# Kernel tuning notes

Hardware: AMD Instinct MI355X
Metric: run time of the kernel (lower is better)

The kernel has to match this reference:

```python
import jax, jax.numpy as jnp
import numpy as np

BETA = 8.0  # cfg.memory.beta (inverse temperature)
EPS = 1e-12  # matches F.normalize default eps


def _l2_normalize(x):
    return x / jnp.maximum(jnp.linalg.norm(x, axis=-1, keepdims=True), EPS)


def setup_inputs() -> dict:
    key = jax.random.key(0)
    k1, k2, k3 = jax.random.split(key, 3)
    embeddings = jax.random.normal(k1, (1024, 128), dtype=jnp.float32)   # queries [B, D]
    keys = jax.random.normal(k2, (100000, 128), dtype=jnp.float32)       # stored patterns [N, D]
    labels = jax.random.randint(k3, (100000,), 0, 1000)                  # class per stored pattern [N]
    return {"embeddings": embeddings, "keys": keys, "labels": labels, "n_classes": 1000}


def reference(embeddings, keys, labels, n_classes):
    # store(): keys normalized (normalize_keys=True); values = one_hot(labels)
    k = _l2_normalize(keys)
    # query(): normalize queries, cosine sims, softmax(beta*sims), weighted value sum
    q = _l2_normalize(embeddings)
    sims = q @ k.T                                   # [B, N]
    weights = jax.nn.softmax(BETA * sims, axis=-1)   # [B, N]
    # weights @ one_hot(labels, C) == segment-sum of weights by key label (same math,
    # avoids materializing the dense [N, C] one-hot value matrix)
    out = jax.ops.segment_sum(weights.T, labels, num_segments=n_classes).T  # [B, C]
    return out
```

## Files before the change

### kernel.cpp

```cpp
#include <hip/hip_runtime.h>
#include <math.h>

typedef _Float16 f16;
typedef _Float16 f16x8 __attribute__((ext_vector_type(8)));
typedef float    f32x16 __attribute__((ext_vector_type(16)));
typedef unsigned int uint;
typedef unsigned short u16;

#define B_Q     1024
#define DIM     128
#define N_KEYS  100000
#define NPAD    102400
#define NGP     (NPAD / 32)
#define GPC     16
#define NCHUNK  (NGP / GPC)
#define N_CLS   1000
#define QSCALE  11.541560327111707f
#define NH      128
#define QGRP    (B_Q / 32)
#define ZFLOATS ((N_CLS + 2) * B_Q)

__global__ void k_hist(const int* __restrict__ labels, uint* __restrict__ hist128) {
    __shared__ uint lh[N_CLS];
    for (int i = threadIdx.x; i < N_CLS; i += blockDim.x) lh[i] = 0;
    __syncthreads();
    const int stride = gridDim.x * blockDim.x;
    for (int i = blockIdx.x * blockDim.x + threadIdx.x; i < N_KEYS; i += stride)
        atomicAdd(&lh[labels[i]], 1u);
    __syncthreads();
    for (int i = threadIdx.x; i < N_CLS; i += blockDim.x)
        hist128[blockIdx.x * N_CLS + i] = lh[i];
}

__global__ __launch_bounds__(1024)
void k_scan(const uint* __restrict__ hist128, uint* __restrict__ cursor) {
    __shared__ uint wtot[16];
    const int t = threadIdx.x;
    const int w = t >> 6, lane = t & 63;
    uint v = 0;
    if (t < N_CLS)
        for (int b = 0; b < NH; ++b) v += hist128[b * N_CLS + t];
    uint s = v;
    #pragma unroll
    for (int o = 1; o < 64; o <<= 1) {
        const uint x = __shfl_up(s, o);
        if (lane >= o) s += x;
    }
    if (lane == 63) wtot[w] = s;
    __syncthreads();
    if (w == 0) {
        uint ws = (lane < 16) ? wtot[lane] : 0;
        #pragma unroll
        for (int o = 1; o < 16; o <<= 1) {
            const uint x = __shfl_up(ws, o);
            if (lane >= o) ws += x;
        }
        if (lane < 16) wtot[lane] = ws;
    }
    __syncthreads();
    const uint prefix = (w > 0) ? wtot[w - 1] : 0;
    if (t < N_CLS) cursor[t] = prefix + s - v;
}

__global__ void k_perm(const int* __restrict__ labels, uint* __restrict__ cursor,
                       int* __restrict__ src, u16* __restrict__ kcls) {
    const int n = blockIdx.x * blockDim.x + threadIdx.x;
    if (n >= NPAD) return;
    if (n < N_KEYS) {
        const int lab = labels[n];
        const int pos = (int)atomicAdd(&cursor[lab], 1u);
        src[pos]  = n;
        kcls[pos] = (u16)lab;
    } else {
        src[n]  = -1;
        kcls[n] = (u16)N_CLS;
    }
}

__global__ __launch_bounds__(256)
void k_gather(const float* __restrict__ qm, const float* __restrict__ km,
              const int* __restrict__ src, const u16* __restrict__ kcls,
              f16* __restrict__ kf2, f16* __restrict__ qf2,
              int* __restrict__ meta, float* __restrict__ zbase) {
    __shared__ float ssq[8][32];
    __shared__ float scale[32];
    const int g = blockIdx.x;
    const int t = threadIdx.x;
    const int r = t & 31;
    const int p = t >> 5;
    const bool isq = g >= NGP;

    {
        const int zi = g * 256 + t;
        if (zi < ZFLOATS / 4)
            ((float4*)zbase)[zi] = float4{0.f, 0.f, 0.f, 0.f};
    }

    if (!isq && t < 64) {
        const int  cl = kcls[g * 32 + (t & 31)];
        const int  ca = __shfl(cl, 0);
        const uint dm = (uint)(__ballot(cl != ca) & 0xffffffffull);
        const int  split = dm ? (__ffs(dm) - 1) : 32;
        const int  cb = (split < 32) ? __shfl(cl, split) : ca;
        if (t == 0) meta[g] = ca | (cb << 11) | (split << 22);
    }

    const float* srow;
    if (isq) srow = qm + (size_t)((g - NGP) * 32 + r) * DIM;
    else {
        const int sr = src[g * 32 + r];
        srow = (sr >= 0) ? km + (size_t)sr * DIM : nullptr;
    }

    float4 v[4];
    float ss = 0.0f;
    if (srow) {
        #pragma unroll
        for (int i = 0; i < 4; ++i) {
            v[i] = *(const float4*)(srow + p * 16 + i * 4);
            ss += v[i].x * v[i].x + v[i].y * v[i].y
                + v[i].z * v[i].z + v[i].w * v[i].w;
        }
    } else {
        #pragma unroll
        for (int i = 0; i < 4; ++i) v[i] = float4{0.f, 0.f, 0.f, 0.f};
    }
    ssq[p][r] = ss;
    __syncthreads();
    if (t < 32) {
        float s = 0.0f;
        #pragma unroll
        for (int i = 0; i < 8; ++i) s += ssq[i][t];
        scale[t] = (isq ? QSCALE : 1.0f) / fmaxf(sqrtf(s), 1e-12f);
    }
    __syncthreads();
    const float sc = scale[r];

    const float f[16] = {v[0].x, v[0].y, v[0].z, v[0].w,
                         v[1].x, v[1].y, v[1].z, v[1].w,
                         v[2].x, v[2].y, v[2].z, v[2].w,
                         v[3].x, v[3].y, v[3].z, v[3].w};
    f16x8 h0, h1;
    #pragma unroll
    for (int j = 0; j < 8; ++j) {
        h0[j] = (f16)(f[j]     * sc);
        h1[j] = (f16)(f[j + 8] * sc);
    }
    f16* dst = isq ? qf2 + (size_t)(g - NGP) * 4096
                   : kf2 + (size_t)g * 4096;
    *(f16x8*)(dst + p * 512 +       r * 8) = h0;
    *(f16x8*)(dst + p * 512 + 256 + r * 8) = h1;
}

#define FLUSH2(C) {                                                           \
        const float v0 = racc0 + __shfl_xor(racc0, 32);                       \
        const float v1 = racc1 + __shfl_xor(racc1, 32);                       \
        if ((C) != N_CLS) { tot0 += racc0; tot1 += racc1; }                   \
        if (lhi == 0) {                                                       \
            atomicAdd(&out_t[(size_t)(C) * B_Q + q00 + l31], v0);             \
            atomicAdd(&out_t[(size_t)(C) * B_Q + q01 + l31], v1);             \
        }                                                                     \
    }

#define LOADK(DST, I) {                                                       \
        const f16* _kb = kf2 + (size_t)(g0 + (I)) * 4096 + lane * 8;          \
        _Pragma("unroll")                                                     \
        for (int kk = 0; kk < 8; ++kk) DST[kk] = *(const f16x8*)(_kb + kk * 512); \
    }

#define BODY(KB, I) {                                                         \
        const int m     = __shfl(mv, (I));                                    \
        const int ca    = m & 0x7FF;                                          \
        const int cb    = (m >> 11) & 0x7FF;                                  \
        const int split = m >> 22;                                            \
        f32x16 c0 = {}, c1 = {};                                              \
        _Pragma("unroll")                                                     \
        for (int kk = 0; kk < 8; ++kk) {                                      \
            c0 = __builtin_amdgcn_mfma_f32_32x32x16_f16(KB[kk], Q0[kk], c0, 0, 0, 0); \
            c1 = __builtin_amdgcn_mfma_f32_32x32x16_f16(KB[kk], Q1[kk], c1, 0, 0, 0); \
        }                                                                     \
        if (ca != cur) {                                                      \
            if (cur >= 0) FLUSH2(cur);                                        \
            racc0 = 0.0f; racc1 = 0.0f;                                       \
            cur = ca;                                                         \
        }                                                                     \
        if (split == 32) {                                                    \
            float ga = 0.f, gb = 0.f, gc = 0.f, gd = 0.f;                     \
            _Pragma("unroll")                                                 \
            for (int r = 0; r < 16; r += 2) {                                 \
                ga += __builtin_amdgcn_exp2f(c0[r]);                          \
                gb += __builtin_amdgcn_exp2f(c0[r + 1]);                      \
                gc += __builtin_amdgcn_exp2f(c1[r]);                          \
                gd += __builtin_amdgcn_exp2f(c1[r + 1]);                      \
            }                                                                 \
            racc0 += ga + gb;                                                 \
            racc1 += gc + gd;                                                 \
        } else {                                                              \
            float ga = 0.f, gb = 0.f, gc = 0.f, gd = 0.f;                     \
            float ha = 0.f, hb = 0.f, hc = 0.f, hd = 0.f;                     \
            _Pragma("unroll")                                                 \
            for (int r = 0; r < 16; r += 2) {                                 \
                const int  kr0 = ((r & 3) + 8 * (r >> 2)) + lhi4;             \
                const int  kr1 = (((r + 1) & 3) + 8 * ((r + 1) >> 2)) + lhi4; \
                const float e0  = __builtin_amdgcn_exp2f(c0[r]);              \
                const float e0b = __builtin_amdgcn_exp2f(c0[r + 1]);          \
                const float e1  = __builtin_amdgcn_exp2f(c1[r]);              \
                const float e1b = __builtin_amdgcn_exp2f(c1[r + 1]);          \
                const bool inA0 = kr0 < split;                                \
                const bool inA1 = kr1 < split;                                \
                ga += inA0 ? e0  : 0.0f;  ha += inA0 ? 0.0f : e0;             \
                gb += inA1 ? e0b : 0.0f;  hb += inA1 ? 0.0f : e0b;            \
                gc += inA0 ? e1  : 0.0f;  hc += inA0 ? 0.0f : e1;             \
                gd += inA1 ? e1b : 0.0f;  hd += inA1 ? 0.0f : e1b;            \
            }                                                                 \
            racc0 += ga + gb;                                                 \
            racc1 += gc + gd;                                                 \
            FLUSH2(cur);                                                      \
            racc0 = ha + hb;                                                  \
            racc1 = hc + hd;                                                  \
            cur = cb;                                                         \
        }                                                                     \
    }

__global__ __launch_bounds__(64)
void class_gemm8(const f16* __restrict__ kf2, const f16* __restrict__ qf2,
                 const int* __restrict__ meta, float* __restrict__ out_t,
                 float* __restrict__ qtot) {
    const int lane = threadIdx.x & 63;
    const int l31  = lane & 31;
    const int lhi  = lane >> 5;
    const int lhi4 = lhi << 2;

    const int b     = blockIdx.x;
    const int xcd   = b & 7;
    const int u     = b >> 3;
    const int chunk = xcd * (NCHUNK / 8) + (u >> 4);
    const int qquad = (u >> 2) & 3;
    const int wsub  = u & 3;
    const int g0    = chunk * GPC;

    f16x8 Q0[8], Q1[8];
    {
        const f16* qa = qf2 + (size_t)(qquad * 8 + wsub * 2) * 4096 + lane * 8;
        #pragma unroll
        for (int kk = 0; kk < 8; ++kk) {
            Q0[kk] = *(const f16x8*)(qa + kk * 512);
            Q1[kk] = *(const f16x8*)(qa + 4096 + kk * 512);
        }
    }
    const int q00 = qquad * 256 + wsub * 64;
    const int q01 = q00 + 32;

    const int mv = meta[g0 + (lane & 15)];

    float racc0 = 0.0f, racc1 = 0.0f;
    float tot0  = 0.0f, tot1  = 0.0f;
    int cur = -1;

    f16x8 K0[8], K1[8];
    LOADK(K0, 0);
    #pragma unroll 1
    for (int ii = 0; ii < GPC / 2; ++ii) {
        const int i0 = 2 * ii, i1 = 2 * ii + 1;
        LOADK(K1, i1);
        BODY(K0, i0);
        if (ii + 1 < GPC / 2) LOADK(K0, i1 + 1);
        BODY(K1, i1);
    }
    if (cur >= 0) FLUSH2(cur);

    {
        const float t0 = tot0 + __shfl_xor(tot0, 32);
        const float t1 = tot1 + __shfl_xor(tot1, 32);
        if (lhi == 0) {
            atomicAdd(&qtot[q00 + l31], t0);
            atomicAdd(&qtot[q01 + l31], t1);
        }
    }
}

__global__ __launch_bounds__(256)
void k_norm_t(const float* __restrict__ out_t, const float* __restrict__ qtot,
              float* __restrict__ out) {
    __shared__ float tile[64 * 65];
    __shared__ float invq[64];
    const int tid  = threadIdx.x;
    const int w    = tid >> 6;
    const int lane = tid & 63;
    const int q0   = blockIdx.x * 64;
    const int c0   = blockIdx.y * 64;

    if (tid < 64) invq[tid] = 1.0f / qtot[q0 + tid];

    #pragma unroll
    for (int i = 0; i < 16; ++i) {
        const int cidx = c0 + w * 16 + i;
        const float v = (cidx < N_CLS) ? out_t[(size_t)cidx * B_Q + q0 + lane] : 0.0f;
        tile[lane * 65 + w * 16 + i] = v;
    }
    __syncthreads();
    #pragma unroll
    for (int j = 0; j < 16; ++j) {
        const int r    = w * 16 + j;
        const int cidx = c0 + lane;
        if (cidx < N_CLS)
            out[(size_t)(q0 + r) * N_CLS + cidx] = tile[r * 65 + lane] * invq[r];
    }
}

extern "C" void kernel_launch(void* const* d_in, const int* in_sizes, int n_in,
                              void* d_out, int out_size, void* d_ws, size_t ws_size,
                              hipStream_t stream) {
    const float* qm     = (const float*)d_in[0];
    const float* km     = (const float*)d_in[1];
    const int*   labels = (const int*)d_in[2];
    float* out = (float*)d_out;

    char* p = (char*)d_ws;
    f16*   kf2     = (f16*)p;   p += (size_t)NPAD * DIM * 2;
    f16*   qf2     = (f16*)p;   p += (size_t)B_Q * DIM * 2;
    float* out_t   = (float*)p; p += (size_t)N_CLS * B_Q * 4;
    float* sink    = (float*)p; p += (size_t)B_Q * 4;
    float* qtot    = (float*)p; p += (size_t)B_Q * 4;
    uint*  cursor  = (uint*)p;  p += N_CLS * 4;
    u16*   kcls    = (u16*)p;   p += (size_t)NPAD * 2;
    int*   meta    = (int*)p;   p += (size_t)NGP * 4;
    int*   src     = (int*)p;   p += (size_t)NPAD * 4;
    (void)sink;
    uint*  hist128 = (uint*)out_t;

    hipLaunchKernelGGL(k_hist, dim3(NH), dim3(256), 0, stream, labels, hist128);
    hipLaunchKernelGGL(k_scan, dim3(1), dim3(1024), 0, stream, hist128, cursor);
    hipLaunchKernelGGL(k_perm, dim3(NPAD / 256), dim3(256), 0, stream,
                       labels, cursor, src, kcls);
    hipLaunchKernelGGL(k_gather, dim3(NGP + QGRP), dim3(256), 0, stream,
                       qm, km, src, kcls, kf2, qf2, meta, out_t);

    hipLaunchKernelGGL(class_gemm8, dim3(16 * NCHUNK), dim3(64), 0, stream,
                       kf2, qf2, meta, out_t, qtot);

    hipLaunchKernelGGL(k_norm_t, dim3(B_Q / 64, (N_CLS + 63) / 64), dim3(256), 0, stream,
                       out_t, qtot, out);
}
```

Measured before the change: 103.0 us.

## Halve key-group chunk size, fully unroll, and defer class merge after MFMA loop

Key groups per chunk drop from 16 to 8, which doubles the grid of the class GEMM kernel. The loop is fully unrolled into a straight-line load/compute schedule. The branchy per-group exp/accumulate with interleaved atomic flushes is replaced by a branch-free split sum that stores lo/hi partials in registers. The class-run merge and atomic flushes then run in a separate pass after all MFMAs finish, so the MFMA pipeline no longer stalls on divergent flush code. The cost is more atomics from the doubled chunk count, which means more partial flushes per class boundary, plus higher register use for the partial arrays.

```diff
diff --git a/kernel.cpp b/kernel.cpp
--- a/kernel.cpp
+++ b/kernel.cpp
@@ -12,7 +12,7 @@
 #define N_KEYS  100000
 #define NPAD    102400
 #define NGP     (NPAD / 32)
-#define GPC     16
+#define GPC     8
 #define NCHUNK  (NGP / GPC)
 #define N_CLS   1000
 #define QSCALE  11.541560327111707f
@@ -95,7 +95,6 @@
         if (zi < ZFLOATS / 4)
             ((float4*)zbase)[zi] = float4{0.f, 0.f, 0.f, 0.f};
     }
-
     if (!isq && t < 64) {
         const int  cl = kcls[g * 32 + (t & 31)];
         const int  ca = __shfl(cl, 0);
@@ -169,61 +168,52 @@
     }
 
 #define BODY(KB, I) {                                                         \
-        const int m     = __shfl(mv, (I));                                    \
-        const int ca    = m & 0x7FF;                                          \
-        const int cb    = (m >> 11) & 0x7FF;                                  \
-        const int split = m >> 22;                                            \
+        const int split = __shfl(mv, (I)) >> 22;                              \
         f32x16 c0 = {}, c1 = {};                                              \
         _Pragma("unroll")                                                     \
         for (int kk = 0; kk < 8; ++kk) {                                      \
             c0 = __builtin_amdgcn_mfma_f32_32x32x16_f16(KB[kk], Q0[kk], c0, 0, 0, 0); \
             c1 = __builtin_amdgcn_mfma_f32_32x32x16_f16(KB[kk], Q1[kk], c1, 0, 0, 0); \
         }                                                                     \
+        float la = 0.f, lb = 0.f, lc = 0.f, ld = 0.f;                         \
+        float ta = 0.f, tb = 0.f, tc = 0.f, td = 0.f;                         \
+        _Pragma("unroll")                                                     \
+        for (int r = 0; r < 16; r += 2) {                                     \
+            const int  kr0 = ((r & 3) + 8 * (r >> 2)) + lhi4;                 \
+            const int  kr1 = (((r + 1) & 3) + 8 * ((r + 1) >> 2)) + lhi4;     \
+            const float e0  = __builtin_amdgcn_exp2f(c0[r]);                  \
+            const float e0b = __builtin_amdgcn_exp2f(c0[r + 1]);              \
+            const float e1  = __builtin_amdgcn_exp2f(c1[r]);                  \
+            const float e1b = __builtin_amdgcn_exp2f(c1[r + 1]);              \
+            ta += e0;  tb += e0b;  tc += e1;  td += e1b;                      \
+            la += (kr0 < split) ? e0  : 0.0f;                                 \
+            lb += (kr1 < split) ? e0b : 0.0f;                                 \
+            lc += (kr0 < split) ? e1  : 0.0f;                                 \
+            ld += (kr1 < split) ? e1b : 0.0f;                                 \
+        }                                                                     \
+        lo0[(I)] = la + lb;  hi0[(I)] = (ta + tb) - (la + lb);                \
+        lo1[(I)] = lc + ld;  hi1[(I)] = (tc + td) - (lc + ld);                \
+    }
+
+#define MERGE(I) {                                                            \
+        const int m     = __shfl(mv, (I));                                    \
+        const int ca    = m & 0x7FF;                                          \
+        const int cb    = (m >> 11) & 0x7FF;                                  \
+        const int split = m >> 22;                                            \
         if (ca != cur) {                                                      \
             if (cur >= 0) FLUSH2(cur);                                        \
-            racc0 = 0.0f; racc1 = 0.0f;                                       \
-            cur = ca;                                                         \
-        }                                                                     \
-        if (split == 32) {                                                    \
-            float ga = 0.f, gb = 0.f, gc = 0.f, gd = 0.f;                     \
-            _Pragma("unroll")                                                 \
-            for (int r = 0; r < 16; r += 2) {                                 \
-                ga += __builtin_amdgcn_exp2f(c0[r]);                          \
-                gb += __builtin_amdgcn_exp2f(c0[r + 1]);                      \
-                gc += __builtin_amdgcn_exp2f(c1[r]);                          \
-                gd += __builtin_amdgcn_exp2f(c1[r + 1]);                      \
-            }                                                                 \
-            racc0 += ga + gb;                                                 \
-            racc1 += gc + gd;                                                 \
-        } else {                                                              \
-            float ga = 0.f, gb = 0.f, gc = 0.f, gd = 0.f;                     \
-            float ha = 0.f, hb = 0.f, hc = 0.f, hd = 0.f;                     \
-            _Pragma("unroll")                                                 \
-            for (int r = 0; r < 16; r += 2) {                                 \
-                const int  kr0 = ((r & 3) + 8 * (r >> 2)) + lhi4;             \
-                const int  kr1 = (((r + 1) & 3) + 8 * ((r + 1) >> 2)) + lhi4; \
-                const float e0  = __builtin_amdgcn_exp2f(c0[r]);              \
-                const float e0b = __builtin_amdgcn_exp2f(c0[r + 1]);          \
-                const float e1  = __builtin_amdgcn_exp2f(c1[r]);              \
-                const float e1b = __builtin_amdgcn_exp2f(c1[r + 1]);          \
-                const bool inA0 = kr0 < split;                                \
-                const bool inA1 = kr1 < split;                                \
-                ga += inA0 ? e0  : 0.0f;  ha += inA0 ? 0.0f : e0;             \
-                gb += inA1 ? e0b : 0.0f;  hb += inA1 ? 0.0f : e0b;            \
-                gc += inA0 ? e1  : 0.0f;  hc += inA0 ? 0.0f : e1;             \
-                gd += inA1 ? e1b : 0.0f;  hd += inA1 ? 0.0f : e1b;            \
-            }                                                                 \
-            racc0 += ga + gb;                                                 \
-            racc1 += gc + gd;                                                 \
+            racc0 = 0.0f; racc1 = 0.0f; cur = ca;                             \
+        }                                                                     \
+        racc0 += lo0[(I)]; racc1 += lo1[(I)];                                 \
+        if (split < 32) {                                                     \
             FLUSH2(cur);                                                      \
-            racc0 = ha + hb;                                                  \
-            racc1 = hc + hd;                                                  \
+            racc0 = hi0[(I)]; racc1 = hi1[(I)];                               \
             cur = cb;                                                         \
         }                                                                     \
     }
 
 __global__ __launch_bounds__(64)
-void class_gemm8(const f16* __restrict__ kf2, const f16* __restrict__ qf2,
+void class_gemm9(const f16* __restrict__ kf2, const f16* __restrict__ qf2,
                  const int* __restrict__ meta, float* __restrict__ out_t,
                  float* __restrict__ qtot) {
     const int lane = threadIdx.x & 63;
@@ -251,22 +241,27 @@
     const int q00 = qquad * 256 + wsub * 64;
     const int q01 = q00 + 32;
 
-    const int mv = meta[g0 + (lane & 15)];
+    const int mv = meta[g0 + (lane & (GPC - 1))];
+
+    float lo0[GPC], hi0[GPC], lo1[GPC], hi1[GPC];
+
+    f16x8 K0[8], K1[8];
+    LOADK(K0, 0);
+    LOADK(K1, 1);
+    BODY(K0, 0); LOADK(K0, 2);
+    BODY(K1, 1); LOADK(K1, 3);
+    BODY(K0, 2); LOADK(K0, 4);
+    BODY(K1, 3); LOADK(K1, 5);
+    BODY(K0, 4); LOADK(K0, 6);
+    BODY(K1, 5); LOADK(K1, 7);
+    BODY(K0, 6);
+    BODY(K1, 7);
 
     float racc0 = 0.0f, racc1 = 0.0f;
     float tot0  = 0.0f, tot1  = 0.0f;
     int cur = -1;
-
-    f16x8 K0[8], K1[8];
-    LOADK(K0, 0);
-    #pragma unroll 1
-    for (int ii = 0; ii < GPC / 2; ++ii) {
-        const int i0 = 2 * ii, i1 = 2 * ii + 1;
-        LOADK(K1, i1);
-        BODY(K0, i0);
-        if (ii + 1 < GPC / 2) LOADK(K0, i1 + 1);
-        BODY(K1, i1);
-    }
+    MERGE(0); MERGE(1); MERGE(2); MERGE(3);
+    MERGE(4); MERGE(5); MERGE(6); MERGE(7);
     if (cur >= 0) FLUSH2(cur);
 
     {
@@ -336,7 +331,7 @@
     hipLaunchKernelGGL(k_gather, dim3(NGP + QGRP), dim3(256), 0, stream,
                        qm, km, src, kcls, kf2, qf2, meta, out_t);
 
-    hipLaunchKernelGGL(class_gemm8, dim3(16 * NCHUNK), dim3(64), 0, stream,
+    hipLaunchKernelGGL(class_gemm9, dim3(16 * NCHUNK), dim3(64), 0, stream,
                        kf2, qf2, meta, out_t, qtot);
 
     hipLaunchKernelGGL(k_norm_t, dim3(B_Q / 64, (N_CLS + 63) / 64), dim3(256), 0, stream,
```

New measurement: 142.8 us. 38.7% more time.
